# Optimization experiments

Hardware: AMD Instinct MI355X
Metric: run time of the kernel (lower is better)

Reference implementation:

```python
import jax, jax.numpy as jnp
import numpy as np
import math

B = 1024
INPUT_SHAPE = (8, 8, 8, 8)
OUTPUT_SHAPE = (8, 8, 8, 8)
RANK_SHAPE = (2, 2, 2, 2)
BLOCK_NUM = 4
OUTPUT_SIZE = int(np.prod(OUTPUT_SHAPE))
CORE_SIZE = int(np.prod(RANK_SHAPE))


def setup_inputs() -> dict:
    key = jax.random.key(0)
    k1, k2, k3 = jax.random.split(key, 3)
    stdv = 1.0 / math.sqrt(OUTPUT_SIZE)  # reset_parameters: uniform(-stdv, stdv)
    inputs = jax.random.normal(k1, (B, int(np.prod(INPUT_SHAPE))), dtype=jnp.float32)
    # core_block{b}: shape rank_shape; factor{j}_block{b}: shape (I_j, O_j, R_j)
    cores = jax.random.uniform(k2, (BLOCK_NUM,) + RANK_SHAPE, minval=-stdv, maxval=stdv, dtype=jnp.float32)
    factors = jax.random.uniform(
        k3, (BLOCK_NUM, len(RANK_SHAPE), INPUT_SHAPE[0], OUTPUT_SHAPE[0], RANK_SHAPE[0]),
        minval=-stdv, maxval=stdv, dtype=jnp.float32)
    return {"inputs": inputs, "cores": cores, "factors": factors}


def reference(inputs, cores, factors):
    Bn = inputs.shape[0]
    # view(-1, *input_shape) then permute(0, n, n-1, ..., 1)
    x = inputs.reshape(Bn, *INPUT_SHAPE)
    x = jnp.transpose(x, (0, 4, 3, 2, 1))  # [B, i3, i2, i1, i0]
    res = jnp.zeros((Bn, OUTPUT_SIZE), dtype=inputs.dtype)
    for b in range(BLOCK_NUM):
        cal = x
        factor_offset = 1
        for j in range(len(RANK_SHAPE)):
            f = factors[b, j]            # (I, J, R)
            I, J, R = f.shape
            cal = cal.reshape(-1, I) @ f.reshape(I, J * R)
            cal = cal.reshape(Bn * factor_offset, -1, J * R)
            cal = jnp.transpose(cal, (0, 2, 1))
            factor_offset *= J
        # contract with core flattened row-major (exactly as core.view(core_size, -1))
        cal = cal.reshape(-1, CORE_SIZE) @ cores[b].reshape(CORE_SIZE, 1)
        res = res + cal.reshape(Bn, -1)
    return res
```

## Files before the change

kernel.cpp:

```cpp
#include <hip/hip_runtime.h>
#include <hip/hip_bf16.h>
#include <stdint.h>

typedef __attribute__((ext_vector_type(8))) __bf16 bf16x8;
typedef __attribute__((ext_vector_type(4))) float f32x4;
typedef __attribute__((ext_vector_type(8))) unsigned short u16x8;

__device__ __forceinline__ unsigned short f2bf(float f) {
    unsigned u = __builtin_bit_cast(unsigned, f);
    return (unsigned short)((u + 0x7fffu + ((u >> 16) & 1u)) >> 16);
}

__device__ __forceinline__ void glds16(const void* g, void* l) {
    __builtin_amdgcn_global_load_lds(
        (const __attribute__((address_space(1))) unsigned int*)(uintptr_t)g,
        (__attribute__((address_space(3))) unsigned int*)l, 16, 0, 0);
}

#define VMCNT(n) asm volatile("s_waitcnt vmcnt(" #n ")" ::: "memory")
#define BAR()                                  \
    do {                                       \
        asm volatile("" ::: "memory");         \
        __builtin_amdgcn_s_barrier();          \
        asm volatile("" ::: "memory");         \
    } while (0)

__global__ __launch_bounds__(256) void prep_slabs(const float* __restrict__ factors,
                                                  const float* __restrict__ cores,
                                                  unsigned short* __restrict__ Aslab,
                                                  unsigned short* __restrict__ Bslab) {
    int idx = blockIdx.x * 256 + threadIdx.x;
    int e = idx & 65535;
    int grp = e >> 12;
    int m = (e >> 4) & 255;
    int k = e & 15;
    int b = k >> 2, q = k & 3, r0 = q >> 1, r1 = q & 1;
    int base = (e >> 4) * 32;
    if (idx < 65536) {
        int o01 = grp * 4 + (m >> 6), a01 = m & 63;
        int o0 = o01 >> 3, o1 = o01 & 7, a0 = a01 >> 3, a1 = a01 & 7;
        float v = factors[b*512 +   0 + a0*16 + o0*2 + r0]
                * factors[b*512 + 128 + a1*16 + o1*2 + r1];
        Aslab[base + k] = f2bf(v);
        Aslab[base + k + 16] = 0;
    } else {
        int o23 = grp * 4 + (m >> 6), a23 = m & 63;
        int o2 = o23 >> 3, o3 = o23 & 7, a2 = a23 >> 3, a3 = a23 & 7;
        float s = 0.f;
#pragma unroll
        for (int r2 = 0; r2 < 2; ++r2)
#pragma unroll
            for (int r3 = 0; r3 < 2; ++r3)
                s += factors[b*512 + 256 + a2*16 + o2*2 + r2]
                   * factors[b*512 + 384 + a3*16 + o3*2 + r3]
                   * cores[b*16 + r3*8 + r2*4 + r1*2 + r0];
        Bslab[base + k] = f2bf(s);
        Bslab[base + k + 16] = 0;
    }
}

__global__ __launch_bounds__(256) void cvt_bf16(const float4* __restrict__ in,
                                                ushort4* __restrict__ out) {
    int i = blockIdx.x * 256 + threadIdx.x;
    float4 v = in[i];
    ushort4 o;
    o.x = f2bf(v.x); o.y = f2bf(v.y); o.z = f2bf(v.z); o.w = f2bf(v.w);
    out[i] = o;
}

__global__ __launch_bounds__(256) void build_w2(const unsigned short* __restrict__ Aslab,
                                                const unsigned short* __restrict__ Bslab,
                                                unsigned short* __restrict__ Wt) {
    __shared__ unsigned short As2[256 * 40];
    __shared__ unsigned short Bs2[256 * 40];
    __shared__ unsigned short lbuf[4 * 64 * 72];
    const int tid = threadIdx.x, lane = tid & 63, w = tid >> 6;
    const int bo = blockIdx.x >> 4, bn4 = blockIdx.x & 15;

    const u16x8* srcA = (const u16x8*)(Aslab + ((size_t)bo * 256 + tid) * 32);
    const u16x8* srcB = (const u16x8*)(Bslab + ((size_t)bn4 * 256 + tid) * 32);
#pragma unroll
    for (int i = 0; i < 4; ++i) {
        *(u16x8*)&As2[tid * 40 + i * 8] = srcA[i];
        *(u16x8*)&Bs2[tid * 40 + i * 8] = srcB[i];
    }
    __syncthreads();

    const int fr = lane & 15, fh = lane >> 4;
    bf16x8 af[4];
#pragma unroll
    for (int mf = 0; mf < 4; ++mf)
        af[mf] = *(const bf16x8*)&As2[(w * 64 + mf * 16 + fr) * 40 + fh * 8];

    for (int wn = 0; wn < 4; ++wn) {
        f32x4 acc[4][4] = {};
        bf16x8 bf_[4];
#pragma unroll
        for (int nf = 0; nf < 4; ++nf)
            bf_[nf] = *(const bf16x8*)&Bs2[(wn * 64 + nf * 16 + fr) * 40 + fh * 8];
#pragma unroll
        for (int mf = 0; mf < 4; ++mf)
#pragma unroll
            for (int nf = 0; nf < 4; ++nf)
                acc[mf][nf] = __builtin_amdgcn_mfma_f32_16x16x32_bf16(
                    af[mf], bf_[nf], acc[mf][nf], 0, 0, 0);
#pragma unroll
        for (int mf = 0; mf < 4; ++mf)
#pragma unroll
            for (int nf = 0; nf < 4; ++nf)
#pragma unroll
                for (int j = 0; j < 4; ++j)
                    lbuf[w * 4608 + (mf * 16 + fh * 4 + j) * 72 + nf * 16 + fr] =
                        f2bf(acc[mf][nf][j]);
        const int o = (bo * 4 + w) * 64 + bn4 * 4 + wn;
        unsigned short* dst = Wt + (size_t)o * 4096;
#pragma unroll
        for (int i = 0; i < 8; ++i) {
            int c = i * 64 + lane;
            *(u16x8*)&dst[c * 8] =
                *(const u16x8*)&lbuf[w * 4608 + (c >> 3) * 72 + (c & 7) * 8];
        }
    }
}

__global__ __launch_bounds__(256) void gemm_bt(const unsigned short* __restrict__ A,
                                               const unsigned short* __restrict__ Bt,
                                               float* __restrict__ C) {
    constexpr int K = 4096;
    constexpr int N = 4096;
    constexpr int BK = 64;
    constexpr int NT = K / BK;
    __shared__ alignas(16) char lds[4][32768];
    const int tid = threadIdx.x;
    const int lane = tid & 63, w = tid >> 6;
    const int wm = w >> 1, wn = w & 1;
    const int xcd = blockIdx.x & 7, idx = blockIdx.x >> 3;
    const int bn = xcd * 4 + (idx & 3);
    const int bm = idx >> 2;

    const unsigned short* gA[4]; const unsigned short* gB[4];
    int lAoff[4], lBoff[4];
#pragma unroll
    for (int i = 0; i < 4; ++i) {
        int cs = w * 256 + i * 64 + lane;
        int row = cs >> 3;
        int c = (cs & 7) ^ ((row >> 1) & 7);
        gA[i] = A  + (size_t)(bm * 128 + row) * K + c * 8;
        gB[i] = Bt + (size_t)(bn * 128 + row) * K + c * 8;
        lAoff[i] = (w * 256 + i * 64) * 16;
        lBoff[i] = 16384 + (w * 256 + i * 64) * 16;
    }

#define STAGE(buf, kt)                                            \
    do {                                                          \
        _Pragma("unroll")                                         \
        for (int i = 0; i < 4; ++i) glds16(gA[i] + (kt), &lds[buf][lAoff[i]]); \
        _Pragma("unroll")                                         \
        for (int i = 0; i < 4; ++i) glds16(gB[i] + (kt), &lds[buf][lBoff[i]]); \
    } while (0)

    const int fr = lane & 15, fh = lane >> 4;
    const int sk = (fr >> 1) & 7;
    int aoff[2][4], boff[2][4];
#pragma unroll
    for (int kk = 0; kk < 2; ++kk)
#pragma unroll
        for (int m = 0; m < 4; ++m) {
            aoff[kk][m] = (wm * 64 + m * 16 + fr) * 128 + (((kk * 4 + fh) ^ sk) << 4);
            boff[kk][m] = 16384 + (wn * 64 + m * 16 + fr) * 128 + (((kk * 4 + fh) ^ sk) << 4);
        }

    f32x4 acc[4][4] = {};

#define COMPUTE(buf)                                                          \
    do {                                                                      \
        const char* base = &lds[buf][0];                                      \
        bf16x8 af[2][4], bfr[2][4];                                           \
        _Pragma("unroll")                                                     \
        for (int kk = 0; kk < 2; ++kk)                                        \
            _Pragma("unroll")                                                 \
            for (int m = 0; m < 4; ++m) {                                     \
                af[kk][m]  = *(const bf16x8*)(base + aoff[kk][m]);            \
                bfr[kk][m] = *(const bf16x8*)(base + boff[kk][m]);            \
            }                                                                 \
        _Pragma("unroll")                                                     \
        for (int kk = 0; kk < 2; ++kk)                                        \
            _Pragma("unroll")                                                 \
            for (int m = 0; m < 4; ++m)                                       \
                _Pragma("unroll")                                             \
                for (int n = 0; n < 4; ++n)                                   \
                    acc[m][n] = __builtin_amdgcn_mfma_f32_16x16x32_bf16(      \
                        af[kk][m], bfr[kk][n], acc[m][n], 0, 0, 0);           \
    } while (0)

    STAGE(0, 0);
    STAGE(1, BK);
    for (int t = 0; t < NT - 2; ++t) {
        STAGE((t + 2) & 3, (t + 2) * BK);
        VMCNT(16);
        BAR();
        COMPUTE(t & 3);
        BAR();
    }
    VMCNT(8);  BAR(); COMPUTE((NT - 2) & 3); BAR();
    VMCNT(0);  BAR(); COMPUTE((NT - 1) & 3);

    const int crow0 = bm * 128 + wm * 64 + fh * 4;
    const int ccol0 = bn * 128 + wn * 64 + fr;
#pragma unroll
    for (int m = 0; m < 4; ++m)
#pragma unroll
        for (int n = 0; n < 4; ++n)
#pragma unroll
            for (int j = 0; j < 4; ++j)
                C[(size_t)(crow0 + m * 16 + j) * N + (ccol0 + n * 16)] = acc[m][n][j];
#undef STAGE
#undef COMPUTE
}

extern "C" void kernel_launch(void* const* d_in, const int* in_sizes, int n_in,
                              void* d_out, int out_size, void* d_ws, size_t ws_size,
                              hipStream_t stream) {
    const float* inputs  = (const float*)d_in[0];
    const float* cores   = (const float*)d_in[1];
    const float* factors = (const float*)d_in[2];
    float* out = (float*)d_out;

    char* ws = (char*)d_ws;
    unsigned short* xb    = (unsigned short*)ws;
    unsigned short* Wt    = (unsigned short*)(ws + (8u << 20));
    unsigned short* Aslab = (unsigned short*)(ws + (40u << 20));
    unsigned short* Bslab = Aslab + 131072;

    prep_slabs<<<512, 256, 0, stream>>>(factors, cores, Aslab, Bslab);
    cvt_bf16<<<4096, 256, 0, stream>>>((const float4*)inputs, (ushort4*)xb);
    build_w2<<<256, 256, 0, stream>>>(Aslab, Bslab, Wt);
    gemm_bt<<<256, 256, 0, stream>>>(xb, Wt, out);
}
```

Baseline: 76.42 us.

## Use 256x256 tiles with split-K and atomic accumulation in GEMM

Result: slower. 107.9 us (+41.2%).

```diff
diff --git a/kernel.cpp b/kernel.cpp
--- a/kernel.cpp
+++ b/kernel.cpp
@@ -123,97 +123,106 @@
     }
 }
 
-__global__ __launch_bounds__(256) void gemm_bt(const unsigned short* __restrict__ A,
-                                               const unsigned short* __restrict__ Bt,
-                                               float* __restrict__ C) {
+__global__ __launch_bounds__(256) void zero_f32(float4* __restrict__ p, int n4) {
+    int i = blockIdx.x * 256 + threadIdx.x;
+    int stride = gridDim.x * 256;
+    for (; i < n4; i += stride) p[i] = float4{0.f, 0.f, 0.f, 0.f};
+}
+
+__global__ __launch_bounds__(512, 2) void gemm_bt8(const unsigned short* __restrict__ A,
+                                                   const unsigned short* __restrict__ Bt,
+                                                   float* __restrict__ C) {
     constexpr int K = 4096;
     constexpr int N = 4096;
     constexpr int BK = 64;
-    constexpr int NT = K / BK;
-    __shared__ alignas(16) char lds[4][32768];
+    constexpr int KCH = 1024;
+    constexpr int NT = KCH / BK;
+    __shared__ alignas(16) char lds[2][65536];
     const int tid = threadIdx.x;
-    const int lane = tid & 63, w = tid >> 6;
-    const int wm = w >> 1, wn = w & 1;
-    const int xcd = blockIdx.x & 7, idx = blockIdx.x >> 3;
-    const int bn = xcd * 4 + (idx & 3);
-    const int bm = idx >> 2;
+    const int lane = tid & 63, wid = tid >> 6;
+    const int wr = wid >> 2, wc = wid & 3;
+    const int xcd = blockIdx.x & 7, r = blockIdx.x >> 3;
+    const int bn = xcd * 2 + (r & 1);
+    const int bm = (r >> 1) & 3;
+    const int ks = r >> 3;
 
     const unsigned short* gA[4]; const unsigned short* gB[4];
     int lAoff[4], lBoff[4];
 #pragma unroll
     for (int i = 0; i < 4; ++i) {
-        int cs = w * 256 + i * 64 + lane;
+        int cs = i * 512 + tid;
         int row = cs >> 3;
         int c = (cs & 7) ^ ((row >> 1) & 7);
-        gA[i] = A  + (size_t)(bm * 128 + row) * K + c * 8;
-        gB[i] = Bt + (size_t)(bn * 128 + row) * K + c * 8;
-        lAoff[i] = (w * 256 + i * 64) * 16;
-        lBoff[i] = 16384 + (w * 256 + i * 64) * 16;
-    }
-
-#define STAGE(buf, kt)                                            \
-    do {                                                          \
-        _Pragma("unroll")                                         \
-        for (int i = 0; i < 4; ++i) glds16(gA[i] + (kt), &lds[buf][lAoff[i]]); \
-        _Pragma("unroll")                                         \
-        for (int i = 0; i < 4; ++i) glds16(gB[i] + (kt), &lds[buf][lBoff[i]]); \
+        gA[i] = A  + (size_t)(bm * 256 + row) * K + ks * KCH + c * 8;
+        gB[i] = Bt + (size_t)(bn * 256 + row) * K + ks * KCH + c * 8;
+        lAoff[i] = i * 8192 + wid * 1024;
+        lBoff[i] = 32768 + i * 8192 + wid * 1024;
+    }
+
+#define STAGE(buf, kt)                                                        \
+    do {                                                                      \
+        _Pragma("unroll")                                                     \
+        for (int i = 0; i < 4; ++i) glds16(gA[i] + (kt), &lds[buf][lAoff[i]]);\
+        _Pragma("unroll")                                                     \
+        for (int i = 0; i < 4; ++i) glds16(gB[i] + (kt), &lds[buf][lBoff[i]]);\
     } while (0)
 
     const int fr = lane & 15, fh = lane >> 4;
     const int sk = (fr >> 1) & 7;
-    int aoff[2][4], boff[2][4];
-#pragma unroll
-    for (int kk = 0; kk < 2; ++kk)
-#pragma unroll
-        for (int m = 0; m < 4; ++m) {
-            aoff[kk][m] = (wm * 64 + m * 16 + fr) * 128 + (((kk * 4 + fh) ^ sk) << 4);
-            boff[kk][m] = 16384 + (wn * 64 + m * 16 + fr) * 128 + (((kk * 4 + fh) ^ sk) << 4);
-        }
-
-    f32x4 acc[4][4] = {};
+    int aoff[2], boff[2];
+#pragma unroll
+    for (int kk = 0; kk < 2; ++kk) {
+        aoff[kk] = (wr * 128 + fr) * 128 + (((kk * 4 + fh) ^ sk) << 4);
+        boff[kk] = 32768 + (wc * 64 + fr) * 128 + (((kk * 4 + fh) ^ sk) << 4);
+    }
+
+    f32x4 acc[8][4] = {};
 
 #define COMPUTE(buf)                                                          \
     do {                                                                      \
         const char* base = &lds[buf][0];                                      \
-        bf16x8 af[2][4], bfr[2][4];                                           \
         _Pragma("unroll")                                                     \
-        for (int kk = 0; kk < 2; ++kk)                                        \
+        for (int kk = 0; kk < 2; ++kk) {                                      \
+            bf16x8 bf4[4], af8[8];                                            \
             _Pragma("unroll")                                                 \
-            for (int m = 0; m < 4; ++m) {                                     \
-                af[kk][m]  = *(const bf16x8*)(base + aoff[kk][m]);            \
-                bfr[kk][m] = *(const bf16x8*)(base + boff[kk][m]);            \
-            }                                                                 \
-        _Pragma("unroll")                                                     \
-        for (int kk = 0; kk < 2; ++kk)                                        \
+            for (int n = 0; n < 4; ++n)                                       \
+                bf4[n] = *(const bf16x8*)(base + boff[kk] + n * 2048);        \
             _Pragma("unroll")                                                 \
-            for (int m = 0; m < 4; ++m)                                       \
+            for (int m = 0; m < 8; ++m)                                       \
+                af8[m] = *(const bf16x8*)(base + aoff[kk] + m * 2048);        \
+            __builtin_amdgcn_s_setprio(1);                                    \
+            _Pragma("unroll")                                                 \
+            for (int m = 0; m < 8; ++m)                                       \
                 _Pragma("unroll")                                             \
                 for (int n = 0; n < 4; ++n)                                   \
                     acc[m][n] = __builtin_amdgcn_mfma_f32_16x16x32_bf16(      \
-                        af[kk][m], bfr[kk][n], acc[m][n], 0, 0, 0);           \
+                        af8[m], bf4[n], acc[m][n], 0, 0, 0);                  \
+            __builtin_amdgcn_s_setprio(0);                                    \
+        }                                                                     \
     } while (0)
 
     STAGE(0, 0);
-    STAGE(1, BK);
-    for (int t = 0; t < NT - 2; ++t) {
-        STAGE((t + 2) & 3, (t + 2) * BK);
-        VMCNT(16);
+    for (int t = 0; t < NT - 1; ++t) {
+        STAGE((t + 1) & 1, (t + 1) * BK);
+        VMCNT(8);
         BAR();
-        COMPUTE(t & 3);
+        COMPUTE(t & 1);
         BAR();
     }
-    VMCNT(8);  BAR(); COMPUTE((NT - 2) & 3); BAR();
-    VMCNT(0);  BAR(); COMPUTE((NT - 1) & 3);
-
-    const int crow0 = bm * 128 + wm * 64 + fh * 4;
-    const int ccol0 = bn * 128 + wn * 64 + fr;
-#pragma unroll
-    for (int m = 0; m < 4; ++m)
+    VMCNT(0);
+    BAR();
+    COMPUTE((NT - 1) & 1);
+
+    const int crow0 = bm * 256 + wr * 128 + fh * 4;
+    const int ccol0 = bn * 256 + wc * 64 + fr;
+#pragma unroll
+    for (int m = 0; m < 8; ++m)
 #pragma unroll
         for (int n = 0; n < 4; ++n)
 #pragma unroll
             for (int j = 0; j < 4; ++j)
-                C[(size_t)(crow0 + m * 16 + j) * N + (ccol0 + n * 16)] = acc[m][n][j];
+                atomicAdd(&C[(size_t)(crow0 + m * 16 + j) * N + (ccol0 + n * 16)],
+                          acc[m][n][j]);
 #undef STAGE
 #undef COMPUTE
 }
@@ -235,5 +244,6 @@
     prep_slabs<<<512, 256, 0, stream>>>(factors, cores, Aslab, Bslab);
     cvt_bf16<<<4096, 256, 0, stream>>>((const float4*)inputs, (ushort4*)xb);
     build_w2<<<256, 256, 0, stream>>>(Aslab, Bslab, Wt);
-    gemm_bt<<<256, 256, 0, stream>>>(xb, Wt, out);
-}
+    zero_f32<<<2048, 256, 0, stream>>>((float4*)out, out_size / 4);
+    gemm_bt8<<<256, 512, 0, stream>>>(xb, Wt, out);
+}
```
